# Kernel optimization log

Measured on AMD Instinct MI355X. Metric: run time of the kernel, lower is better.

## Reference

```python
import jax, jax.numpy as jnp
import numpy as np

N_NODES = 100000
N_EDGES = 1600000
IN_FEAT = 50
HIDDEN = 64
N_CLASSES = 41


def setup_inputs() -> dict:
    key = jax.random.key(0)
    ks = jax.random.split(key, 8)
    x = jax.random.normal(ks[0], (N_NODES, IN_FEAT), dtype=jnp.float32)
    W1_l = jax.random.normal(ks[1], (IN_FEAT, HIDDEN), dtype=jnp.float32) * (1.0 / np.sqrt(IN_FEAT))
    W1_r = jax.random.normal(ks[2], (IN_FEAT, HIDDEN), dtype=jnp.float32) * (1.0 / np.sqrt(IN_FEAT))
    b1 = jnp.zeros((HIDDEN,), dtype=jnp.float32)
    W2_l = jax.random.normal(ks[3], (HIDDEN, N_CLASSES), dtype=jnp.float32) * (1.0 / np.sqrt(HIDDEN))
    W2_r = jax.random.normal(ks[4], (HIDDEN, N_CLASSES), dtype=jnp.float32) * (1.0 / np.sqrt(HIDDEN))
    b2 = jnp.zeros((N_CLASSES,), dtype=jnp.float32)
    src = jax.random.randint(ks[5], (N_EDGES,), 0, N_NODES, dtype=jnp.int64 if jax.config.jax_enable_x64 else jnp.int32)
    dst = jax.random.randint(ks[6], (N_EDGES,), 0, N_NODES, dtype=jnp.int64 if jax.config.jax_enable_x64 else jnp.int32)
    return {"x": x, "W1_l": W1_l, "W1_r": W1_r, "b1": b1,
            "W2_l": W2_l, "W2_r": W2_r, "b2": b2, "src": src, "dst": dst}


def _sage_conv(h, src, dst, W_l, W_r, b):
    # sum-aggregate neighbor features (message from src -> dst), then dense transform
    agg = jax.ops.segment_sum(h[src], dst, num_segments=N_NODES)  # [N, F]
    return agg @ W_l + h @ W_r + b


def reference(x, W1_l, W1_r, b1, W2_l, W2_r, b2, src, dst):
    h = _sage_conv(x, src, dst, W1_l, W1_r, b1)
    h = jax.nn.relu(h)
    # dropout is identity in eval mode
    o = _sage_conv(h, src, dst, W2_l, W2_r, b2)
    return jax.nn.log_softmax(o, axis=1)
```

## Files before the change

### kernel.cpp

```cpp
#include <hip/hip_runtime.h>
#include <hip/hip_bf16.h>
#include <math.h>

#define N_NODES   100000
#define N_EDGES   1600000
#define IN_FEAT   50
#define HIDDEN    64
#define N_CLASSES 41
#define NC48      48
#define N_TILES   (N_NODES / 16)
#define XW        56
#define XQ        7

#define NPB   200
#define NBUK  (N_NODES / NPB)
#define SLOTS 4096
#define BEPT  16
#define BA_BLOCKS ((N_EDGES + 256 * BEPT - 1) / (256 * BEPT))
#define SCAP  4096

#define PACKX_BLOCKS (N_NODES * XW / 256)
#define PW_BLOCKS    28

typedef __attribute__((ext_vector_type(8))) _Float16 half8;
typedef __attribute__((ext_vector_type(4))) float   float4v;

union f16pk { _Float16 h[2]; unsigned u; };

__device__ __forceinline__ int clampidx(int i) {
  return ((unsigned)i < (unsigned)N_NODES) ? i : 0;
}

__device__ __forceinline__ int clampoff(int v) {
  return ((unsigned)v <= (unsigned)N_EDGES) ? v : 0;
}

__device__ __forceinline__ void acc8(float* acc, half8 u, float one) {
#pragma unroll
  for (int t = 0; t < 8; ++t) acc[t] = fmaf((float)u[t], one, acc[t]);
}

__device__ __forceinline__ void accf8(float* acc, uint2 u) {
  auto p0 = __builtin_amdgcn_cvt_pk_f32_fp8(u.x, 0);
  auto p1 = __builtin_amdgcn_cvt_pk_f32_fp8(u.x, 1);
  auto p2 = __builtin_amdgcn_cvt_pk_f32_fp8(u.y, 0);
  auto p3 = __builtin_amdgcn_cvt_pk_f32_fp8(u.y, 1);
  acc[0] += p0[0]; acc[1] += p0[1];
  acc[2] += p1[0]; acc[3] += p1[1];
  acc[4] += p2[0]; acc[5] += p2[1];
  acc[6] += p3[0]; acc[7] += p3[1];
}

__global__ __launch_bounds__(256) void prep_kernel(
    const float* __restrict__ x, _Float16* __restrict__ xh,
    const float* __restrict__ W1l, const float* __restrict__ W1r,
    const float* __restrict__ W2l, const float* __restrict__ W2r,
    unsigned* __restrict__ wt1l, unsigned* __restrict__ wt1r,
    unsigned* __restrict__ wt2l, unsigned* __restrict__ wt2r,
    int* __restrict__ wcur2, int* __restrict__ start) {
  if (blockIdx.x < PACKX_BLOCKS) {
    int i = blockIdx.x * 256 + threadIdx.x;
    int node = i / XW, c = i - node * XW;
    xh[i] = (c < IN_FEAT) ? (_Float16)x[node * IN_FEAT + c] : (_Float16)0.f;
    return;
  }
  int tid = threadIdx.x;
  if (blockIdx.x == PACKX_BLOCKS) {
    wcur2[tid] = 0; wcur2[256 + tid] = 0;
    if (tid == 0) start[N_NODES] = N_EDGES;
  }
  int i = (blockIdx.x - PACKX_BLOCKS) * 256 + tid;
  f16pk pk;
  if (i < 2048 * 2) {
    int which = i >> 11, j = i & 2047;
    int n = j >> 5, kp = j & 31;
    const float* W = which ? W1r : W1l;
    int k0 = 2 * kp, k1 = 2 * kp + 1;
    pk.h[0] = (_Float16)((k0 < IN_FEAT) ? W[k0 * HIDDEN + n] : 0.f);
    pk.h[1] = (_Float16)((k1 < IN_FEAT) ? W[k1 * HIDDEN + n] : 0.f);
    (which ? wt1r : wt1l)[j] = pk.u;
  } else if (i < 4096 + 2 * 1536) {
    int j = i - 4096;
    int which = (j >= 1536), jj = which ? j - 1536 : j;
    int n = jj >> 5, kp = jj & 31;
    const float* W = which ? W2r : W2l;
    pk.h[0] = (_Float16)((n < N_CLASSES) ? W[(2 * kp) * N_CLASSES + n] : 0.f);
    pk.h[1] = (_Float16)((n < N_CLASSES) ? W[(2 * kp + 1) * N_CLASSES + n] : 0.f);
    (which ? wt2r : wt2l)[jj] = pk.u;
  }
}

__global__ __launch_bounds__(256) void bucketA_kernel(
    const int* __restrict__ src, const int* __restrict__ dst,
    int* __restrict__ wcur2, int* __restrict__ pairs) {
  __shared__ int lcnt[NBUK];
  __shared__ int lbase[NBUK];
  int tid = threadIdx.x;
  for (int i = tid; i < NBUK; i += 256) { lcnt[i] = 0; lbase[i] = 0; }
  __syncthreads();

  int base = blockIdx.x * (256 * BEPT);
  int pk[BEPT], w[BEPT], rk[BEPT];
#pragma unroll
  for (int k = 0; k < BEPT; ++k) {
    int e = base + k * 256 + tid;
    rk[k] = -1;
    if (e < N_EDGES) {
      int sv = clampidx(src[e]);
      int d = clampidx(dst[e]);
      w[k] = (unsigned)d / (unsigned)NPB;
      pk[k] = (sv << 8) | (d - w[k] * NPB);
      rk[k] = atomicAdd(&lcnt[w[k]], 1);
    }
  }
  __syncthreads();
  for (int i = tid; i < NBUK; i += 256)
    if (lcnt[i]) lbase[i] = atomicAdd(&wcur2[i], lcnt[i]);
  __syncthreads();
#pragma unroll
  for (int k = 0; k < BEPT; ++k) {
    if (rk[k] >= 0) {
      unsigned rel = (unsigned)(lbase[w[k]] + rk[k]);
      if (rel < (unsigned)SLOTS) pairs[w[k] * SLOTS + (int)rel] = pk[k];
    }
  }
}

__global__ __launch_bounds__(256) void sort2_kernel(
    const int* __restrict__ pairs, const int* __restrict__ wcur2,
    int* __restrict__ start, int* __restrict__ ssrc) {
  __shared__ int obuf[SCAP];
  __shared__ int lhist[NPB];
  __shared__ int lcur[NPB];
  __shared__ int lscan[256];
  __shared__ int lohi[2];
  int b = blockIdx.x;
  int nbase = b * NPB;
  int tid = threadIdx.x;
  {
    int i0 = 2 * tid, i1 = 2 * tid + 1;
    int a0 = (i0 < NBUK) ? min(max(wcur2[i0], 0), SLOTS) : 0;
    int a1 = (i1 < NBUK) ? min(max(wcur2[i1], 0), SLOTS) : 0;
    int s = a0 + a1;
    lscan[tid] = s;
    __syncthreads();
    for (int off = 1; off < 256; off <<= 1) {
      int t = (tid >= off) ? lscan[tid - off] : 0;
      __syncthreads();
      lscan[tid] += t;
      __syncthreads();
    }
    int excl = lscan[tid] - s;
    if (i0 == b) { lohi[0] = excl;      lohi[1] = a0; }
    if (i1 == b) { lohi[0] = excl + a0; lohi[1] = a1; }
  }
  for (int i = tid; i < NPB; i += 256) lhist[i] = 0;
  __syncthreads();
  int glo = lohi[0];
  int ne  = lohi[1];
  int plo = b * SLOTS;
  for (int i = tid; i < ne; i += 256) {
    unsigned li = (unsigned)pairs[plo + i] & 255u;
    if (li < (unsigned)NPB) atomicAdd(&lhist[li], 1);
  }
  __syncthreads();
  int hv = (tid < NPB) ? lhist[tid] : 0;
  lscan[tid] = hv;
  __syncthreads();
  for (int off = 1; off < 256; off <<= 1) {
    int t = (tid >= off) ? lscan[tid - off] : 0;
    __syncthreads();
    lscan[tid] += t;
    __syncthreads();
  }
  if (tid < NPB) {
    int excl = lscan[tid] - hv;
    lcur[tid] = excl;
    unsigned sidx = (unsigned)(nbase + tid);
    if (sidx < (unsigned)N_NODES) start[sidx] = glo + excl;
  }
  __syncthreads();
  for (int i = tid; i < ne; i += 256) {
    int p = pairs[plo + i];
    unsigned li = (unsigned)p & 255u;
    if (li < (unsigned)NPB) {
      int pos = atomicAdd(&lcur[li], 1);
      if ((unsigned)pos < (unsigned)SCAP) obuf[pos] = (int)((unsigned)p >> 8);
    }
  }
  __syncthreads();
  for (int i = tid; i < ne; i += 256) {
    unsigned gi = (unsigned)(glo + i);
    if (gi < (unsigned)N_EDGES) ssrc[gi] = obuf[i];
  }
}

__global__ __launch_bounds__(256) void g1mlp_kernel(
    const half8* __restrict__ xq,
    const int* __restrict__ start, const int* __restrict__ ssrc,
    const unsigned* __restrict__ wt1l, const unsigned* __restrict__ wt1r,
    const unsigned* __restrict__ wt2l, const unsigned* __restrict__ wt2r,
    const float* __restrict__ b1, const float* __restrict__ b2,
    unsigned char* __restrict__ hlf8, _Float16* __restrict__ opart16,
    float one) {
  __shared__ float aggF[16][68];
  __shared__ float sH[16][68];
  int tile = blockIdx.x;
  int wv = __builtin_amdgcn_readfirstlane(threadIdx.x >> 6);
  int lane = threadIdx.x & 63;
  int r = lane >> 3, q = lane & 7;
  bool qOK = (q < XQ);

  int nb = tile * 16 + wv * 4;
  int st[5];
#pragma unroll
  for (int k = 0; k < 5; ++k) st[k] = clampoff(start[nb + k]);
  int iv[4];
#pragma unroll
  for (int k = 0; k < 4; ++k) {
    int cnt = st[k + 1] - st[k]; if (cnt > 64) cnt = 64;
    iv[k] = (lane < cnt) ? ssrc[st[k] + lane] : 0;
  }
#pragma unroll
  for (int k = 0; k < 4; ++k) {
    float accA[8] = {0.f, 0.f, 0.f, 0.f, 0.f, 0.f, 0.f, 0.f};
    float accB[8] = {0.f, 0.f, 0.f, 0.f, 0.f, 0.f, 0.f, 0.f};
    int s0 = st[k], s1 = st[k + 1];
    int idxv = iv[k];
    for (int base = s0; base < s1; base += 64) {
      int cnt = s1 - base;
      if (cnt > 64) cnt = 64;
      if (base != s0) idxv = (lane < cnt) ? ssrc[base + lane] : 0;
      int j = 0;
      for (; j + 16 <= cnt; j += 16) {
        int iA = clampidx(__shfl(idxv, j + r));
        int iB = clampidx(__shfl(idxv, j + 8 + r));
        if (qOK) {
          acc8(accA, xq[iA * XQ + q], one);
          acc8(accB, xq[iB * XQ + q], one);
        }
      }
      for (; j + 8 <= cnt; j += 8) {
        int iA = clampidx(__shfl(idxv, j + r));
        if (qOK) acc8(accA, xq[iA * XQ + q], one);
      }
      if (j < cnt) {
        int nrem = cnt - j;
        int iA = clampidx(__shfl(idxv, j + r));
        if (r < nrem && qOK) acc8(accA, xq[iA * XQ + q], one);
      }
    }
#pragma unroll
    for (int t = 0; t < 8; ++t) accA[t] += accB[t];
#pragma unroll
    for (int off = 8; off <= 32; off <<= 1) {
#pragma unroll
      for (int t = 0; t < 8; ++t) accA[t] += __shfl_xor(accA[t], off);
    }
    if (r == 0) {
      int nl = wv * 4 + k;
#pragma unroll
      for (int t = 0; t < 8; ++t) aggF[nl][q * 8 + t] = accA[t];
    }
  }
  __syncthreads();

  int m = lane & 15, quad = lane >> 4;

  half8 Aa[2], Ax[2];
#pragma unroll
  for (int s = 0; s < 2; ++s) {
    const float* pa = &aggF[m][s * 32 + quad * 8];
    half8 A;
#pragma unroll
    for (int jj = 0; jj < 8; ++jj) A[jj] = (_Float16)pa[jj];
    Aa[s] = A;
    int qq = s * 4 + quad;
    half8 X = {0, 0, 0, 0, 0, 0, 0, 0};
    if (qq < XQ) X = xq[(tile * 16 + m) * XQ + qq];
    Ax[s] = X;
  }

  {
    int n = wv * 16 + m;
    half8 Bl0 = *(const half8*)(wt1l + n * 32 + quad * 4);
    half8 Bl1 = *(const half8*)(wt1l + n * 32 + 16 + quad * 4);
    half8 Br0 = *(const half8*)(wt1r + n * 32 + quad * 4);
    half8 Br1 = *(const half8*)(wt1r + n * 32 + 16 + quad * 4);
    float4v acc1 = {0.f, 0.f, 0.f, 0.f};
    acc1 = __builtin_amdgcn_mfma_f32_16x16x32_f16(Aa[0], Bl0, acc1, 0, 0, 0);
    acc1 = __builtin_amdgcn_mfma_f32_16x16x32_f16(Aa[1], Bl1, acc1, 0, 0, 0);
    acc1 = __builtin_amdgcn_mfma_f32_16x16x32_f16(Ax[0], Br0, acc1, 0, 0, 0);
    acc1 = __builtin_amdgcn_mfma_f32_16x16x32_f16(Ax[1], Br1, acc1, 0, 0, 0);
    float bv = b1[n];
#pragma unroll
    for (int rr = 0; rr < 4; ++rr) {
      sH[quad * 4 + rr][n] = fmaxf(acc1[rr] + bv, 0.f);
    }
  }
  __syncthreads();

  if (wv >= 3) return;
  half8 Ah[2];
#pragma unroll
  for (int s = 0; s < 2; ++s) {
    const float* pr = &sH[m][s * 32 + quad * 8];
    half8 A;
#pragma unroll
    for (int jj = 0; jj < 8; ++jj) A[jj] = (_Float16)pr[jj];
    Ah[s] = A;
  }
  {
    int n = wv * 16 + m;
    half8 Cl0 = *(const half8*)(wt2l + n * 32 + quad * 4);
    half8 Cl1 = *(const half8*)(wt2l + n * 32 + 16 + quad * 4);
    half8 Cr0 = *(const half8*)(wt2r + n * 32 + quad * 4);
    half8 Cr1 = *(const half8*)(wt2r + n * 32 + 16 + quad * 4);
    float4v acc2 = {0.f, 0.f, 0.f, 0.f};
    float4v acc3 = {0.f, 0.f, 0.f, 0.f};
    acc2 = __builtin_amdgcn_mfma_f32_16x16x32_f16(Ah[0], Cl0, acc2, 0, 0, 0);
    acc2 = __builtin_amdgcn_mfma_f32_16x16x32_f16(Ah[1], Cl1, acc2, 0, 0, 0);
    acc3 = __builtin_amdgcn_mfma_f32_16x16x32_f16(Ah[0], Cr0, acc3, 0, 0, 0);
    acc3 = __builtin_amdgcn_mfma_f32_16x16x32_f16(Ah[1], Cr1, acc3, 0, 0, 0);
    float bv = (n < N_CLASSES) ? b2[n] : 0.f;
#pragma unroll
    for (int rr = 0; rr < 4; ++rr) {
      int row = tile * 16 + quad * 4 + rr;
      int v8 = __builtin_amdgcn_cvt_pk_fp8_f32(acc2[rr], acc2[rr], 0, 0);
      hlf8[row * NC48 + n] = (unsigned char)(v8 & 0xff);
      opart16[row * NC48 + n] = (_Float16)(acc3[rr] + bv);
    }
  }
}

#define AROW 49
__global__ __launch_bounds__(256) void g2tile_kernel(
    const uint2* __restrict__ hq,
    const _Float16* __restrict__ opart16,
    const int* __restrict__ start, const int* __restrict__ ssrc,
    float* __restrict__ out) {
  __shared__ float aggF[16][AROW];
  int tile = blockIdx.x;
  int wv = __builtin_amdgcn_readfirstlane(threadIdx.x >> 6);
  int lane = threadIdx.x & 63;
  int r = lane >> 3, q = lane & 7;
  bool qOK = (q < 6);

  int nb = tile * 16 + wv * 4;
  int st[5];
#pragma unroll
  for (int k = 0; k < 5; ++k) st[k] = clampoff(start[nb + k]);
  int iv[4];
#pragma unroll
  for (int k = 0; k < 4; ++k) {
    int cnt = st[k + 1] - st[k]; if (cnt > 64) cnt = 64;
    iv[k] = (lane < cnt) ? ssrc[st[k] + lane] : 0;
  }
#pragma unroll
  for (int k = 0; k < 4; ++k) {
    float accA[8] = {0.f, 0.f, 0.f, 0.f, 0.f, 0.f, 0.f, 0.f};
    float accB[8] = {0.f, 0.f, 0.f, 0.f, 0.f, 0.f, 0.f, 0.f};
    int s0 = st[k], s1 = st[k + 1];
    int idxv = iv[k];
    for (int base = s0; base < s1; base += 64) {
      int cnt = s1 - base;
      if (cnt > 64) cnt = 64;
      if (base != s0) idxv = (lane < cnt) ? ssrc[base + lane] : 0;
      int j = 0;
      for (; j + 16 <= cnt; j += 16) {
        int iA = clampidx(__shfl(idxv, j + r));
        int iB = clampidx(__shfl(idxv, j + 8 + r));
        if (qOK) {
          accf8(accA, hq[iA * 6 + q]);
          accf8(accB, hq[iB * 6 + q]);
        }
      }
      for (; j + 8 <= cnt; j += 8) {
        int iA = clampidx(__shfl(idxv, j + r));
        if (qOK) accf8(accA, hq[iA * 6 + q]);
      }
      if (j < cnt) {
        int nrem = cnt - j;
        int iA = clampidx(__shfl(idxv, j + r));
        if (r < nrem && qOK) accf8(accA, hq[iA * 6 + q]);
      }
    }
#pragma unroll
    for (int t = 0; t < 8; ++t) accA[t] += accB[t];
#pragma unroll
    for (int off = 8; off <= 32; off <<= 1) {
#pragma unroll
      for (int t = 0; t < 8; ++t) accA[t] += __shfl_xor(accA[t], off);
    }
    if (r == 0 && qOK) {
      int nl = wv * 4 + k;
#pragma unroll
      for (int t = 0; t < 8; ++t) aggF[nl][q * 8 + t] = accA[t];
    }
  }
  __syncthreads();

  if (wv != 0) return;
  int m = lane >> 2, s = lane & 3;
  int node = tile * 16 + m;

  float o[12];
#pragma unroll
  for (int j = 0; j < 12; ++j)
    o[j] = (float)opart16[node * NC48 + s * 12 + j];
  float lmax = -INFINITY;
#pragma unroll
  for (int j = 0; j < 12; ++j) {
    int f = s * 12 + j;
    o[j] += aggF[m][f];
    if (f < N_CLASSES) lmax = fmaxf(lmax, o[j]);
  }
  float vm = lmax;
#pragma unroll
  for (int off = 1; off <= 2; off <<= 1) vm = fmaxf(vm, __shfl_xor(vm, off));
  float lsum = 0.f;
#pragma unroll
  for (int j = 0; j < 12; ++j) {
    int f = s * 12 + j;
    if (f < N_CLASSES) lsum += expf(o[j] - vm);
  }
#pragma unroll
  for (int off = 1; off <= 2; off <<= 1) lsum += __shfl_xor(lsum, off);
  float lse = logf(lsum);
#pragma unroll
  for (int j = 0; j < 12; ++j) {
    int f = s * 12 + j;
    if (f < N_CLASSES) out[node * N_CLASSES + f] = o[j] - vm - lse;
  }
}

extern "C" void kernel_launch(void* const* d_in, const int* in_sizes, int n_in,
                              void* d_out, int out_size, void* d_ws, size_t ws_size,
                              hipStream_t stream) {
  const float* x   = (const float*)d_in[0];
  const float* W1l = (const float*)d_in[1];
  const float* W1r = (const float*)d_in[2];
  const float* b1  = (const float*)d_in[3];
  const float* W2l = (const float*)d_in[4];
  const float* W2r = (const float*)d_in[5];
  const float* b2  = (const float*)d_in[6];
  const int*   src = (const int*)d_in[7];
  const int*   dst = (const int*)d_in[8];
  float* out = (float*)d_out;

  int* counts  = (int*)d_ws;
  int* start   = counts + N_NODES;
  int* cursor  = start + (N_NODES + 1);
  int* partial = cursor + N_NODES;
  int* ssrc    = partial + 64;
  unsigned* wt1l = (unsigned*)(ssrc + N_EDGES);
  unsigned* wt1r = wt1l + 2048;
  unsigned* wt2l = wt1r + 2048;
  unsigned* wt2r = wt2l + 1536;
  uintptr_t pal = ((uintptr_t)(wt2r + 1536) + 255) & ~(uintptr_t)255;
  float* opart   = (float*)pal;
  _Float16* xh   = (_Float16*)(opart + (size_t)N_NODES * NC48);
  _Float16* hlh  = xh + (size_t)N_NODES * 64;

  _Float16* xq56    = xh;
  unsigned char* hlf8 = (unsigned char*)hlh;
  _Float16* opart16 = (_Float16*)opart;

  int* wcur2 = counts;

  int* pairs = (int*)opart;

  prep_kernel<<<PACKX_BLOCKS + PW_BLOCKS, 256, 0, stream>>>(
      x, xq56, W1l, W1r, W2l, W2r, wt1l, wt1r, wt2l, wt2r, wcur2, start);
  bucketA_kernel<<<BA_BLOCKS, 256, 0, stream>>>(src, dst, wcur2, pairs);
  sort2_kernel<<<NBUK, 256, 0, stream>>>(pairs, wcur2, start, ssrc);

  g1mlp_kernel<<<N_TILES, 256, 0, stream>>>(
      (const half8*)xq56, start, ssrc, wt1l, wt1r, wt2l, wt2r,
      b1, b2, hlf8, opart16, 1.0f);

  g2tile_kernel<<<N_TILES, 256, 0, stream>>>(
      (const uint2*)hlf8, opart16, start, ssrc, out);
}
```

Measured before the change: 217.7 us.

## Fold input/weight packing into sort kernel and zero counters via memset

The separate prep kernel that converted x and the weights to fp16 is removed. Its work now runs as extra blocks appended to the bucket-sort kernel's grid, so the packing overlaps with the per-bucket sort. The counter zeroing that prep did is replaced by a hipMemsetAsync before bucketA. This cuts one kernel launch and lets the packing share the GPU with the sort, but adds a memset node and makes the sort launch a larger mixed-role grid.

New measurement: 211.5 us (median of 2 runs). 2.8% less time.

```diff
diff --git a/kernel.cpp b/kernel.cpp
--- a/kernel.cpp
+++ b/kernel.cpp
@@ -51,45 +51,6 @@
   acc[6] += p3[0]; acc[7] += p3[1];
 }
 
-__global__ __launch_bounds__(256) void prep_kernel(
-    const float* __restrict__ x, _Float16* __restrict__ xh,
-    const float* __restrict__ W1l, const float* __restrict__ W1r,
-    const float* __restrict__ W2l, const float* __restrict__ W2r,
-    unsigned* __restrict__ wt1l, unsigned* __restrict__ wt1r,
-    unsigned* __restrict__ wt2l, unsigned* __restrict__ wt2r,
-    int* __restrict__ wcur2, int* __restrict__ start) {
-  if (blockIdx.x < PACKX_BLOCKS) {
-    int i = blockIdx.x * 256 + threadIdx.x;
-    int node = i / XW, c = i - node * XW;
-    xh[i] = (c < IN_FEAT) ? (_Float16)x[node * IN_FEAT + c] : (_Float16)0.f;
-    return;
-  }
-  int tid = threadIdx.x;
-  if (blockIdx.x == PACKX_BLOCKS) {
-    wcur2[tid] = 0; wcur2[256 + tid] = 0;
-    if (tid == 0) start[N_NODES] = N_EDGES;
-  }
-  int i = (blockIdx.x - PACKX_BLOCKS) * 256 + tid;
-  f16pk pk;
-  if (i < 2048 * 2) {
-    int which = i >> 11, j = i & 2047;
-    int n = j >> 5, kp = j & 31;
-    const float* W = which ? W1r : W1l;
-    int k0 = 2 * kp, k1 = 2 * kp + 1;
-    pk.h[0] = (_Float16)((k0 < IN_FEAT) ? W[k0 * HIDDEN + n] : 0.f);
-    pk.h[1] = (_Float16)((k1 < IN_FEAT) ? W[k1 * HIDDEN + n] : 0.f);
-    (which ? wt1r : wt1l)[j] = pk.u;
-  } else if (i < 4096 + 2 * 1536) {
-    int j = i - 4096;
-    int which = (j >= 1536), jj = which ? j - 1536 : j;
-    int n = jj >> 5, kp = jj & 31;
-    const float* W = which ? W2r : W2l;
-    pk.h[0] = (_Float16)((n < N_CLASSES) ? W[(2 * kp) * N_CLASSES + n] : 0.f);
-    pk.h[1] = (_Float16)((n < N_CLASSES) ? W[(2 * kp + 1) * N_CLASSES + n] : 0.f);
-    (which ? wt2r : wt2l)[jj] = pk.u;
-  }
-}
-
 __global__ __launch_bounds__(256) void bucketA_kernel(
     const int* __restrict__ src, const int* __restrict__ dst,
     int* __restrict__ wcur2, int* __restrict__ pairs) {
@@ -126,17 +87,54 @@
   }
 }
 
-__global__ __launch_bounds__(256) void sort2_kernel(
+__global__ __launch_bounds__(256) void sortprep_kernel(
     const int* __restrict__ pairs, const int* __restrict__ wcur2,
-    int* __restrict__ start, int* __restrict__ ssrc) {
+    int* __restrict__ start, int* __restrict__ ssrc,
+    const float* __restrict__ x, _Float16* __restrict__ xh,
+    const float* __restrict__ W1l, const float* __restrict__ W1r,
+    const float* __restrict__ W2l, const float* __restrict__ W2r,
+    unsigned* __restrict__ wt1l, unsigned* __restrict__ wt1r,
+    unsigned* __restrict__ wt2l, unsigned* __restrict__ wt2r) {
   __shared__ int obuf[SCAP];
   __shared__ int lhist[NPB];
   __shared__ int lcur[NPB];
   __shared__ int lscan[256];
   __shared__ int lohi[2];
+  int tid = threadIdx.x;
+
+  if (blockIdx.x >= NBUK) {
+    int bb = blockIdx.x - NBUK;
+    if (bb < PACKX_BLOCKS) {
+      int i = bb * 256 + tid;
+      int node = i / XW, c = i - node * XW;
+      xh[i] = (c < IN_FEAT) ? (_Float16)x[node * IN_FEAT + c] : (_Float16)0.f;
+      return;
+    }
+    if (bb == PACKX_BLOCKS && tid == 0) start[N_NODES] = N_EDGES;
+    int i = (bb - PACKX_BLOCKS) * 256 + tid;
+    f16pk pk;
+    if (i < 2048 * 2) {
+      int which = i >> 11, j = i & 2047;
+      int n = j >> 5, kp = j & 31;
+      const float* W = which ? W1r : W1l;
+      int k0 = 2 * kp, k1 = 2 * kp + 1;
+      pk.h[0] = (_Float16)((k0 < IN_FEAT) ? W[k0 * HIDDEN + n] : 0.f);
+      pk.h[1] = (_Float16)((k1 < IN_FEAT) ? W[k1 * HIDDEN + n] : 0.f);
+      (which ? wt1r : wt1l)[j] = pk.u;
+    } else if (i < 4096 + 2 * 1536) {
+      int j = i - 4096;
+      int which = (j >= 1536), jj = which ? j - 1536 : j;
+      int n = jj >> 5, kp = jj & 31;
+      const float* W = which ? W2r : W2l;
+      pk.h[0] = (_Float16)((n < N_CLASSES) ? W[(2 * kp) * N_CLASSES + n] : 0.f);
+      pk.h[1] = (_Float16)((n < N_CLASSES) ? W[(2 * kp + 1) * N_CLASSES + n] : 0.f);
+      (which ? wt2r : wt2l)[jj] = pk.u;
+    }
+    return;
+  }
+
   int b = blockIdx.x;
   int nbase = b * NPB;
-  int tid = threadIdx.x;
   {
     int i0 = 2 * tid, i1 = 2 * tid + 1;
     int a0 = (i0 < NBUK) ? min(max(wcur2[i0], 0), SLOTS) : 0;
@@ -470,10 +468,11 @@
 
   int* pairs = (int*)opart;
 
-  prep_kernel<<<PACKX_BLOCKS + PW_BLOCKS, 256, 0, stream>>>(
-      x, xq56, W1l, W1r, W2l, W2r, wt1l, wt1r, wt2l, wt2r, wcur2, start);
+  hipMemsetAsync(wcur2, 0, 512 * sizeof(int), stream);
   bucketA_kernel<<<BA_BLOCKS, 256, 0, stream>>>(src, dst, wcur2, pairs);
-  sort2_kernel<<<NBUK, 256, 0, stream>>>(pairs, wcur2, start, ssrc);
+  sortprep_kernel<<<NBUK + PACKX_BLOCKS + PW_BLOCKS, 256, 0, stream>>>(
+      pairs, wcur2, start, ssrc,
+      x, xq56, W1l, W1r, W2l, W2r, wt1l, wt1r, wt2l, wt2r);
 
   g1mlp_kernel<<<N_TILES, 256, 0, stream>>>(
       (const half8*)xq56, start, ssrc, wt1l, wt1r, wt2l, wt2r,
```
